# Optimization experiments

Measured on AMD Instinct MI355X. Metric: run time of the kernel, lower is better.

Reference implementation:

```python
import jax, jax.numpy as jnp
import numpy as np

MAX_DISP = 4  # displacement range [-4, 4] -> 9x9 = 81 output channels


def setup_inputs() -> dict:
    key = jax.random.key(0)
    k1, k2 = jax.random.split(key)
    B, C, H, W = 8, 128, 128, 256
    tensorFirst = jax.random.normal(k1, (B, C, H, W), dtype=jnp.float32)
    tensorSecond = jax.random.normal(k2, (B, C, H, W), dtype=jnp.float32)
    return {"tensorFirst": tensorFirst, "tensorSecond": tensorSecond}


def reference(tensorFirst, tensorSecond):
    # PWC-Net style correlation: out[b, d, y, x] =
    #   (1/C) * sum_c first[b,c,y,x] * second[b,c,y+dy,x+dx]
    # with zero padding, dy,dx in [-4,4], d = (dy+4)*9 + (dx+4).
    B, C, H, W = tensorFirst.shape
    p = MAX_DISP
    second_pad = jnp.pad(tensorSecond, ((0, 0), (0, 0), (p, p), (p, p)))
    outs = []
    for dy in range(-p, p + 1):
        for dx in range(-p, p + 1):
            shifted = jax.lax.dynamic_slice(
                second_pad, (0, 0, dy + p, dx + p), (B, C, H, W))
            # mean over channels, matching the cupy kernel's /C normalization
            outs.append(jnp.mean(tensorFirst * shifted, axis=1))
    return jnp.stack(outs, axis=1)  # [B, 81, H, W]
```

## Files before the change

kernel.cpp:

```cpp
#include <hip/hip_runtime.h>

#define CC   128
#define HH   128
#define WW   256
#define BB   8
#define HWS  (HH * WW)
#define TH   16
#define TW   64
#define SROWS (TH + 8)
#define SCOLS (TW + 8)
#define STILE (SROWS * SCOLS)
#define NTHR 768

typedef float f4 __attribute__((ext_vector_type(4)));

__global__ __launch_bounds__(NTHR)
void corr_kernel(const float* __restrict__ first,
                 const float* __restrict__ second,
                 float* __restrict__ out)
{
    __shared__ float s_lds[2 * STILE];

    const int tid = threadIdx.x;
    const int g   = tid >> 8;
    const int p   = tid & 255;
    const int r   = p >> 4;
    const int xq  = p & 15;
    const int x0  = xq << 2;

    const int bx = blockIdx.x * TW;
    const int by = blockIdx.y * TH;
    const int b  = blockIdx.z;

    const int y  = by + r;
    const int xg = bx + x0;

    const int i0 = tid;
    const int i1 = tid + NTHR;
    const int i2 = tid + 2 * NTHR;

    const int sr0 = i0 / SCOLS, sc0 = i0 % SCOLS;
    const int sr1 = i1 / SCOLS, sc1 = i1 % SCOLS;
    const int sr2 = i2 / SCOLS, sc2 = i2 % SCOLS;

    const int ys0 = by - 4 + sr0, xs0 = bx - 4 + sc0;
    const int ys1 = by - 4 + sr1, xs1 = bx - 4 + sc1;
    const int ys2 = by - 4 + sr2, xs2 = bx - 4 + sc2;

    const bool v0 = ((unsigned)ys0 < HH) && ((unsigned)xs0 < WW);
    const bool v1 = ((unsigned)ys1 < HH) && ((unsigned)xs1 < WW);
    const bool v2 = (i2 < STILE) && ((unsigned)ys2 < HH) && ((unsigned)xs2 < WW);

    const float* sbase = second + (long)b * CC * HWS;
    int go0 = v0 ? (ys0 * WW + xs0) : 0;
    int go1 = v1 ? (ys1 * WW + xs1) : 0;
    int go2 = v2 ? (ys2 * WW + xs2) : 0;

    float acc[3][9][4];
    #pragma unroll
    for (int a = 0; a < 3; ++a)
        #pragma unroll
        for (int d = 0; d < 9; ++d)
            #pragma unroll
            for (int q = 0; q < 4; ++q)
                acc[a][d][q] = 0.0f;

    {
        float t0 = v0 ? sbase[go0] : 0.0f;
        float t1 = v1 ? sbase[go1] : 0.0f;
        float t2 = v2 ? sbase[go2] : 0.0f;
        s_lds[i0] = t0;
        s_lds[i1] = t1;
        if (i2 < STILE) s_lds[i2] = t2;
    }
    __syncthreads();

    const float* fptr = first + ((long)(b * CC) * HH + y) * WW + xg;

    int cur = 0;
    for (int c = 0; c < CC; ++c) {
        float t0 = 0.0f, t1 = 0.0f, t2 = 0.0f;
        const bool more = (c + 1 < CC);
        if (more) {
            const float* sb = sbase + (c + 1) * HWS;
            t0 = v0 ? sb[go0] : 0.0f;
            t1 = v1 ? sb[go1] : 0.0f;
            t2 = v2 ? sb[go2] : 0.0f;
        }

        f4 fv = *(const f4*)fptr;
        fptr += HWS;

        const float* sb_lds = &s_lds[cur * STILE];
        #pragma unroll
        for (int r3 = 0; r3 < 3; ++r3) {
            const int srow = r + g * 3 + r3;
            const f4* wp = (const f4*)&sb_lds[srow * SCOLS + x0];
            f4 wa = wp[0];
            f4 wb = wp[1];
            f4 wc = wp[2];
            float w[12];
            w[0] = wa[0]; w[1]  = wa[1]; w[2]  = wa[2]; w[3]  = wa[3];
            w[4] = wb[0]; w[5]  = wb[1]; w[6]  = wb[2]; w[7]  = wb[3];
            w[8] = wc[0]; w[9]  = wc[1]; w[10] = wc[2]; w[11] = wc[3];
            #pragma unroll
            for (int dxi = 0; dxi < 9; ++dxi) {
                #pragma unroll
                for (int px = 0; px < 4; ++px) {
                    acc[r3][dxi][px] = fmaf(fv[px], w[dxi + px], acc[r3][dxi][px]);
                }
            }
        }

        if (more) {
            const int nb = (cur ^ 1) * STILE;
            s_lds[nb + i0] = t0;
            s_lds[nb + i1] = t1;
            if (i2 < STILE) s_lds[nb + i2] = t2;
        }
        __syncthreads();
        cur ^= 1;
    }

    const float scale = 1.0f / (float)CC;
    #pragma unroll
    for (int r3 = 0; r3 < 3; ++r3) {
        #pragma unroll
        for (int dxi = 0; dxi < 9; ++dxi) {
            const int d = (g * 3 + r3) * 9 + dxi;
            f4 o;
            o[0] = acc[r3][dxi][0] * scale;
            o[1] = acc[r3][dxi][1] * scale;
            o[2] = acc[r3][dxi][2] * scale;
            o[3] = acc[r3][dxi][3] * scale;
            *(f4*)(out + (long)(b * 81 + d) * HWS + y * WW + xg) = o;
        }
    }
}

extern "C" void kernel_launch(void* const* d_in, const int* in_sizes, int n_in,
                              void* d_out, int out_size, void* d_ws, size_t ws_size,
                              hipStream_t stream) {
    const float* first  = (const float*)d_in[0];
    const float* second = (const float*)d_in[1];
    float* out = (float*)d_out;

    dim3 grid(WW / TW, HH / TH, BB);
    corr_kernel<<<grid, NTHR, 0, stream>>>(first, second, out);
}
```

Measured before the change: 160.2 us.

## Pack two channels as fp16 pairs in LDS and process two channels per iteration

Stores the shifted second-tensor tile in LDS as packed fp16 pairs, two channels per 32-bit word, so each loop iteration handles two channels and the number of barriers is halved. The first tensor stays fp32 and accumulation is still fp32, but the second operand is rounded to fp16 (round toward zero), which reduces precision. It also adds a min-waves launch bound and extra conversion instructions per LDS word, which may add register pressure given the 108 accumulators.

```diff
diff --git a/kernel.cpp b/kernel.cpp
--- a/kernel.cpp
+++ b/kernel.cpp
@@ -11,15 +11,23 @@
 #define SCOLS (TW + 8)
 #define STILE (SROWS * SCOLS)
 #define NTHR 768
+#define NPER (CC / 2)
 
-typedef float f4 __attribute__((ext_vector_type(4)));
+typedef float    f4  __attribute__((ext_vector_type(4)));
+typedef unsigned u4v __attribute__((ext_vector_type(4)));
+typedef __fp16   h2  __attribute__((ext_vector_type(2)));
 
-__global__ __launch_bounds__(NTHR)
+static __device__ __forceinline__ unsigned pack2(float a, float b) {
+    h2 pk = __builtin_amdgcn_cvt_pkrtz(a, b);
+    return __builtin_bit_cast(unsigned, pk);
+}
+
+__global__ __launch_bounds__(NTHR, 3)
 void corr_kernel(const float* __restrict__ first,
                  const float* __restrict__ second,
                  float* __restrict__ out)
 {
-    __shared__ float s_lds[2 * STILE];
+    __shared__ __align__(16) unsigned s_lds[2 * STILE];
 
     const int tid = threadIdx.x;
     const int g   = tid >> 8;
@@ -52,9 +60,9 @@
     const bool v2 = (i2 < STILE) && ((unsigned)ys2 < HH) && ((unsigned)xs2 < WW);
 
     const float* sbase = second + (long)b * CC * HWS;
-    int go0 = v0 ? (ys0 * WW + xs0) : 0;
-    int go1 = v1 ? (ys1 * WW + xs1) : 0;
-    int go2 = v2 ? (ys2 * WW + xs2) : 0;
+    const int go0 = v0 ? (ys0 * WW + xs0) : 0;
+    const int go1 = v1 ? (ys1 * WW + xs1) : 0;
+    const int go2 = v2 ? (ys2 * WW + xs2) : 0;
 
     float acc[3][9][4];
     #pragma unroll
@@ -66,57 +74,63 @@
                 acc[a][d][q] = 0.0f;
 
     {
-        float t0 = v0 ? sbase[go0] : 0.0f;
-        float t1 = v1 ? sbase[go1] : 0.0f;
-        float t2 = v2 ? sbase[go2] : 0.0f;
-        s_lds[i0] = t0;
-        s_lds[i1] = t1;
-        if (i2 < STILE) s_lds[i2] = t2;
+        float a0 = v0 ? sbase[go0] : 0.0f, b0 = v0 ? sbase[go0 + HWS] : 0.0f;
+        float a1 = v1 ? sbase[go1] : 0.0f, b1 = v1 ? sbase[go1 + HWS] : 0.0f;
+        float a2 = v2 ? sbase[go2] : 0.0f, b2 = v2 ? sbase[go2 + HWS] : 0.0f;
+        s_lds[i0] = pack2(a0, b0);
+        s_lds[i1] = pack2(a1, b1);
+        if (i2 < STILE) s_lds[i2] = pack2(a2, b2);
     }
     __syncthreads();
 
     const float* fptr = first + ((long)(b * CC) * HH + y) * WW + xg;
 
     int cur = 0;
-    for (int c = 0; c < CC; ++c) {
-        float t0 = 0.0f, t1 = 0.0f, t2 = 0.0f;
-        const bool more = (c + 1 < CC);
-        if (more) {
-            const float* sb = sbase + (c + 1) * HWS;
-            t0 = v0 ? sb[go0] : 0.0f;
-            t1 = v1 ? sb[go1] : 0.0f;
-            t2 = v2 ? sb[go2] : 0.0f;
-        }
+    for (int it = 0; it < NPER; ++it) {
+        const int ip = (it + 1 < NPER) ? (it + 1) : it;
+        const float* sb = sbase + (long)(2 * ip) * HWS;
+        float t0a = v0 ? sb[go0] : 0.0f, t0b = v0 ? sb[go0 + HWS] : 0.0f;
+        float t1a = v1 ? sb[go1] : 0.0f, t1b = v1 ? sb[go1 + HWS] : 0.0f;
+        float t2a = v2 ? sb[go2] : 0.0f, t2b = v2 ? sb[go2 + HWS] : 0.0f;
 
-        f4 fv = *(const f4*)fptr;
-        fptr += HWS;
+        const float* fpit = fptr + (long)(2 * it) * HWS;
+        f4 f0 = *(const f4*)fpit;
+        f4 f1 = *(const f4*)(fpit + HWS);
 
-        const float* sb_lds = &s_lds[cur * STILE];
+        const unsigned* sb_lds = &s_lds[cur * STILE];
         #pragma unroll
         for (int r3 = 0; r3 < 3; ++r3) {
             const int srow = r + g * 3 + r3;
-            const f4* wp = (const f4*)&sb_lds[srow * SCOLS + x0];
-            f4 wa = wp[0];
-            f4 wb = wp[1];
-            f4 wc = wp[2];
-            float w[12];
-            w[0] = wa[0]; w[1]  = wa[1]; w[2]  = wa[2]; w[3]  = wa[3];
-            w[4] = wb[0]; w[5]  = wb[1]; w[6]  = wb[2]; w[7]  = wb[3];
-            w[8] = wc[0]; w[9]  = wc[1]; w[10] = wc[2]; w[11] = wc[3];
+            const u4v* wp = (const u4v*)&sb_lds[srow * SCOLS + x0];
+            u4v qa = wp[0];
+            u4v qb = wp[1];
+            u4v qc = wp[2];
+            unsigned wu[12] = { qa[0], qa[1], qa[2], qa[3],
+                                qb[0], qb[1], qb[2], qb[3],
+                                qc[0], qc[1], qc[2], qc[3] };
+            float wlo[12], whi[12];
+            #pragma unroll
+            for (int j = 0; j < 12; ++j) {
+                h2 hv = __builtin_bit_cast(h2, wu[j]);
+                wlo[j] = (float)hv[0];
+                whi[j] = (float)hv[1];
+            }
             #pragma unroll
             for (int dxi = 0; dxi < 9; ++dxi) {
                 #pragma unroll
                 for (int px = 0; px < 4; ++px) {
-                    acc[r3][dxi][px] = fmaf(fv[px], w[dxi + px], acc[r3][dxi][px]);
+                    acc[r3][dxi][px] = fmaf(f1[px], whi[dxi + px],
+                                       fmaf(f0[px], wlo[dxi + px],
+                                            acc[r3][dxi][px]));
                 }
             }
         }
 
-        if (more) {
+        if (it + 1 < NPER) {
             const int nb = (cur ^ 1) * STILE;
-            s_lds[nb + i0] = t0;
-            s_lds[nb + i1] = t1;
-            if (i2 < STILE) s_lds[nb + i2] = t2;
+            s_lds[nb + i0] = pack2(t0a, t0b);
+            s_lds[nb + i1] = pack2(t1a, t1b);
+            if (i2 < STILE) s_lds[nb + i2] = pack2(t2a, t2b);
         }
         __syncthreads();
         cur ^= 1;
```

Result: slower. 180.3 us (+12.6%).

## Split dy rows across blocks with 256-thread blocks and XCD-aware block remap

Applied to the files above, without the earlier changes.

Each former 768-thread block handling all 9 dy rows for a tile becomes five 256-thread blocks, each covering two dy rows (the last covers one, with a wasted duplicate row). Every block still loads the full halo tile of the second input and the first-input vector, so global and LDS staging traffic grows about fivefold. In exchange the grid has 1280 blocks instead of 256, and each block holds fewer accumulators, which raises occupancy and fills the GPU better. Block indices are permuted so that blocks sharing the same batch and tile land on the same XCD for L2 reuse.

```diff
diff --git a/kernel.cpp b/kernel.cpp
--- a/kernel.cpp
+++ b/kernel.cpp
@@ -10,11 +10,12 @@
 #define SROWS (TH + 8)
 #define SCOLS (TW + 8)
 #define STILE (SROWS * SCOLS)
-#define NTHR 768
+#define NTHR 256
+#define NSTG 7
 
 typedef float f4 __attribute__((ext_vector_type(4)));
 
-__global__ __launch_bounds__(NTHR)
+__global__ __launch_bounds__(NTHR, 4)
 void corr_kernel(const float* __restrict__ first,
                  const float* __restrict__ second,
                  float* __restrict__ out)
@@ -22,101 +23,100 @@
     __shared__ float s_lds[2 * STILE];
 
     const int tid = threadIdx.x;
-    const int g   = tid >> 8;
-    const int p   = tid & 255;
-    const int r   = p >> 4;
-    const int xq  = p & 15;
-    const int x0  = xq << 2;
+    const int r   = tid >> 4;
+    const int x0  = (tid & 15) << 2;
 
-    const int bx = blockIdx.x * TW;
-    const int by = blockIdx.y * TH;
-    const int b  = blockIdx.z;
+    const int u    = (blockIdx.x & 7) * 160 + (blockIdx.x >> 3);
+    const int b    = u / 160;
+    const int rem  = u - b * 160;
+    const int tile = rem / 5;
+    const int m    = rem - tile * 5;
+    const int xt   = tile & 3;
+    const int yt   = tile >> 2;
 
+    const int d0 = 2 * m;
+    const int d1 = 2 * m + 1;
+
+    const int bx = xt * TW;
+    const int by = yt * TH;
     const int y  = by + r;
     const int xg = bx + x0;
 
-    const int i0 = tid;
-    const int i1 = tid + NTHR;
-    const int i2 = tid + 2 * NTHR;
-
-    const int sr0 = i0 / SCOLS, sc0 = i0 % SCOLS;
-    const int sr1 = i1 / SCOLS, sc1 = i1 % SCOLS;
-    const int sr2 = i2 / SCOLS, sc2 = i2 % SCOLS;
-
-    const int ys0 = by - 4 + sr0, xs0 = bx - 4 + sc0;
-    const int ys1 = by - 4 + sr1, xs1 = bx - 4 + sc1;
-    const int ys2 = by - 4 + sr2, xs2 = bx - 4 + sc2;
-
-    const bool v0 = ((unsigned)ys0 < HH) && ((unsigned)xs0 < WW);
-    const bool v1 = ((unsigned)ys1 < HH) && ((unsigned)xs1 < WW);
-    const bool v2 = (i2 < STILE) && ((unsigned)ys2 < HH) && ((unsigned)xs2 < WW);
+    int  go[NSTG];
+    bool vv[NSTG];
+    #pragma unroll
+    for (int k = 0; k < NSTG; ++k) {
+        const int i  = tid + k * NTHR;
+        const bool ok = (i < STILE);
+        const int sr = i / SCOLS, sc = i - (i / SCOLS) * SCOLS;
+        const int ys = by - 4 + sr, xs = bx - 4 + sc;
+        const bool v = ok && ((unsigned)ys < HH) && ((unsigned)xs < WW);
+        vv[k] = v;
+        go[k] = v ? (ys * WW + xs) : 0;
+    }
 
     const float* sbase = second + (long)b * CC * HWS;
-    int go0 = v0 ? (ys0 * WW + xs0) : 0;
-    int go1 = v1 ? (ys1 * WW + xs1) : 0;
-    int go2 = v2 ? (ys2 * WW + xs2) : 0;
 
-    float acc[3][9][4];
+    float acc[2][9][4];
     #pragma unroll
-    for (int a = 0; a < 3; ++a)
+    for (int a = 0; a < 2; ++a)
         #pragma unroll
         for (int d = 0; d < 9; ++d)
             #pragma unroll
             for (int q = 0; q < 4; ++q)
                 acc[a][d][q] = 0.0f;
 
-    {
-        float t0 = v0 ? sbase[go0] : 0.0f;
-        float t1 = v1 ? sbase[go1] : 0.0f;
-        float t2 = v2 ? sbase[go2] : 0.0f;
-        s_lds[i0] = t0;
-        s_lds[i1] = t1;
-        if (i2 < STILE) s_lds[i2] = t2;
+    #pragma unroll
+    for (int k = 0; k < NSTG; ++k) {
+        const int i = tid + k * NTHR;
+        if (i < STILE) s_lds[i] = vv[k] ? sbase[go[k]] : 0.0f;
     }
     __syncthreads();
 
     const float* fptr = first + ((long)(b * CC) * HH + y) * WW + xg;
 
+    const int srow0 = r + d0;
+    const int srow1 = (d1 < 9) ? (r + d1) : 23;
+
     int cur = 0;
-    for (int c = 0; c < CC; ++c) {
-        float t0 = 0.0f, t1 = 0.0f, t2 = 0.0f;
-        const bool more = (c + 1 < CC);
-        if (more) {
-            const float* sb = sbase + (c + 1) * HWS;
-            t0 = v0 ? sb[go0] : 0.0f;
-            t1 = v1 ? sb[go1] : 0.0f;
-            t2 = v2 ? sb[go2] : 0.0f;
-        }
+    for (int it = 0; it < CC; ++it) {
+        const int ip = (it + 1 < CC) ? (it + 1) : it;
+        const float* sb = sbase + (long)ip * HWS;
+        float t[NSTG];
+        #pragma unroll
+        for (int k = 0; k < NSTG; ++k)
+            t[k] = vv[k] ? sb[go[k]] : 0.0f;
 
         f4 fv = *(const f4*)fptr;
         fptr += HWS;
 
         const float* sb_lds = &s_lds[cur * STILE];
         #pragma unroll
-        for (int r3 = 0; r3 < 3; ++r3) {
-            const int srow = r + g * 3 + r3;
+        for (int dd = 0; dd < 2; ++dd) {
+            const int srow = dd ? srow1 : srow0;
             const f4* wp = (const f4*)&sb_lds[srow * SCOLS + x0];
             f4 wa = wp[0];
             f4 wb = wp[1];
             f4 wc = wp[2];
-            float w[12];
-            w[0] = wa[0]; w[1]  = wa[1]; w[2]  = wa[2]; w[3]  = wa[3];
-            w[4] = wb[0]; w[5]  = wb[1]; w[6]  = wb[2]; w[7]  = wb[3];
-            w[8] = wc[0]; w[9]  = wc[1]; w[10] = wc[2]; w[11] = wc[3];
+            float w[12] = { wa[0], wa[1], wa[2], wa[3],
+                            wb[0], wb[1], wb[2], wb[3],
+                            wc[0], wc[1], wc[2], wc[3] };
             #pragma unroll
             for (int dxi = 0; dxi < 9; ++dxi) {
                 #pragma unroll
                 for (int px = 0; px < 4; ++px) {
-                    acc[r3][dxi][px] = fmaf(fv[px], w[dxi + px], acc[r3][dxi][px]);
+                    acc[dd][dxi][px] = fmaf(fv[px], w[dxi + px], acc[dd][dxi][px]);
                 }
             }
         }
 
-        if (more) {
+        if (it + 1 < CC) {
             const int nb = (cur ^ 1) * STILE;
-            s_lds[nb + i0] = t0;
-            s_lds[nb + i1] = t1;
-            if (i2 < STILE) s_lds[nb + i2] = t2;
+            #pragma unroll
+            for (int k = 0; k < NSTG; ++k) {
+                const int i = tid + k * NTHR;
+                if (i < STILE) s_lds[nb + i] = t[k];
+            }
         }
         __syncthreads();
         cur ^= 1;
@@ -124,16 +124,19 @@
 
     const float scale = 1.0f / (float)CC;
     #pragma unroll
-    for (int r3 = 0; r3 < 3; ++r3) {
-        #pragma unroll
-        for (int dxi = 0; dxi < 9; ++dxi) {
-            const int d = (g * 3 + r3) * 9 + dxi;
-            f4 o;
-            o[0] = acc[r3][dxi][0] * scale;
-            o[1] = acc[r3][dxi][1] * scale;
-            o[2] = acc[r3][dxi][2] * scale;
-            o[3] = acc[r3][dxi][3] * scale;
-            *(f4*)(out + (long)(b * 81 + d) * HWS + y * WW + xg) = o;
+    for (int dd = 0; dd < 2; ++dd) {
+        const int dyi = dd ? d1 : d0;
+        if (dyi < 9) {
+            #pragma unroll
+            for (int dxi = 0; dxi < 9; ++dxi) {
+                f4 o;
+                o[0] = acc[dd][dxi][0] * scale;
+                o[1] = acc[dd][dxi][1] * scale;
+                o[2] = acc[dd][dxi][2] * scale;
+                o[3] = acc[dd][dxi][3] * scale;
+                *(f4*)(out + (long)(b * 81 + dyi * 9 + dxi) * HWS
+                           + (long)y * WW + xg) = o;
+            }
         }
     }
 }
@@ -145,6 +148,5 @@
     const float* second = (const float*)d_in[1];
     float* out = (float*)d_out;
 
-    dim3 grid(WW / TW, HH / TH, BB);
-    corr_kernel<<<grid, NTHR, 0, stream>>>(first, second, out);
+    corr_kernel<<<dim3(1280), dim3(NTHR), 0, stream>>>(first, second, out);
 }
```

New measurement: 245.9 us. +53.6%, slower.
